# Kernel tuning notes

Measured on AMD Instinct MI355X. Metric: run time of the kernel, lower is better.

## Reference

```python
import jax, jax.numpy as jnp
import numpy as np

N = 50000        # nodes
E = 1600000      # edges (avg degree 32)
H = 128          # hidden_channels == num_filters
G = 50           # num_gaussians
L = 5            # num_interactions
CUTOFF = 4.5
VOCAB = 100
LOG2 = float(np.log(2.0))


def setup_inputs() -> dict:
    key = jax.random.key(0)
    ks = jax.random.split(key, 12)
    s = 1.0 / np.sqrt(H)
    sg = 1.0 / np.sqrt(G)
    atomic_numbers = jax.random.randint(ks[0], (N,), 0, VOCAB, dtype=jnp.int32)
    edge_index = jax.random.randint(ks[1], (2, E), 0, N, dtype=jnp.int32)
    edge_attr = jax.random.uniform(ks[2], (E,), dtype=jnp.float32)
    emb = jax.random.normal(ks[3], (VOCAB, H), dtype=jnp.float32) * 0.1
    emb = emb.at[0].set(0.0)  # padding_idx=0
    Wi = jax.random.normal(ks[4], (L, H, H), dtype=jnp.float32) * s
    bi = jnp.zeros((L, H), dtype=jnp.float32)
    Wn = jax.random.normal(ks[5], (L, G, H), dtype=jnp.float32) * sg
    bn = jnp.zeros((L, H), dtype=jnp.float32)
    Wo = jax.random.normal(ks[6], (L, H, H), dtype=jnp.float32) * s
    bo = jnp.zeros((L, H), dtype=jnp.float32)
    Wl = jax.random.normal(ks[7], (L, H, H), dtype=jnp.float32) * s
    bl = jnp.zeros((L, H), dtype=jnp.float32)
    return {"atomic_numbers": atomic_numbers, "edge_index": edge_index,
            "edge_attr": edge_attr, "emb": emb,
            "Wi": Wi, "bi": bi, "Wn": Wn, "bn": bn,
            "Wo": Wo, "bo": bo, "Wl": Wl, "bl": bl}


def _gaussian_smearing(dist):
    offsets = jnp.linspace(0.0, CUTOFF, G, dtype=jnp.float32)
    coeff = -0.5 / (offsets[1] - offsets[0]) ** 2
    return jnp.exp(coeff * (dist[:, None] - offsets[None, :]) ** 2)  # [E, G]


def reference(atomic_numbers, edge_index, edge_attr, emb,
              Wi, bi, Wn, bn, Wo, bo, Wl, bl):
    src, dst = edge_index[0], edge_index[1]
    x = emb[atomic_numbers]                      # [N, H]
    gauss = _gaussian_smearing(edge_attr)        # [E, G]
    C = 0.5 * (jnp.cos(edge_attr * jnp.pi / CUTOFF) + 1.0)  # cosine cutoff [E]
    for l in range(L):
        W = (gauss @ Wn[l] + bn[l]) * C[:, None]   # edge filters [E, H]
        h = x @ Wi[l] + bi[l]                       # [N, H]
        msg = h[src] * W                            # gather + filter [E, H]
        agg = jax.ops.segment_sum(msg, dst, num_segments=N)  # scatter-add [N, H]
        h = agg @ Wo[l] + bo[l]
        h = jax.nn.softplus(h) - LOG2               # shifted softplus
        h = h @ Wl[l] + bl[l]
        x = x + h                                   # residual
    return x
```

## Files before the change

kernel.cpp:

```cpp
#include <hip/hip_runtime.h>
#include <hip/hip_bf16.h>

#define HDIM 128
#define NG 50
#define NL 5
#define TBN 4096
#define CAP 96
#define CAPB 9000
#define CHUNK 8192

static constexpr float CUTOFF_F = 4.5f;
static constexpr float PI_F = 3.14159265358979323846f;
static constexpr float LN2_F = 0.6931471805599453f;

typedef __attribute__((ext_vector_type(8))) short bf16x8;
typedef __attribute__((ext_vector_type(4))) float f32x4;

__device__ __forceinline__ unsigned f2bfbits(float f) {
    unsigned b = __float_as_uint(f);
    return (b + 0x7FFFu + ((b >> 16) & 1u)) >> 16;
}
__device__ __forceinline__ float bflo(unsigned u) { return __uint_as_float(u << 16); }
__device__ __forceinline__ float bfhi(unsigned u) { return __uint_as_float(u & 0xFFFF0000u); }

__device__ __forceinline__ float softplus_shifted(float v) {
    return fmaxf(v, 0.0f) + log1pf(__expf(-fabsf(v))) - LN2_F;
}

__global__ __launch_bounds__(256) void embed_kernel(
    const int* __restrict__ an, const float* __restrict__ emb,
    float* __restrict__ x, int n)
{
    int idx = blockIdx.x * 256 + threadIdx.x;
    int total = n * (HDIM / 4);
    if (idx >= total) return;
    int i = idx >> 5;
    int j = idx & 31;
    int a = an[i];
    reinterpret_cast<float4*>(x)[(size_t)i * 32 + j] =
        reinterpret_cast<const float4*>(emb)[(size_t)a * 32 + j];
}

__global__ __launch_bounds__(256) void prep_weights(
    const float* __restrict__ Wi, const float* __restrict__ Wo,
    const float* __restrict__ Wl, unsigned short* __restrict__ Wt)
{
    int b = blockIdx.x;
    int l = b / 3, m = b % 3;
    const float* src = (m == 0 ? Wi : (m == 1 ? Wo : Wl)) + (size_t)l * HDIM * HDIM;
    unsigned short* dst = Wt + (size_t)b * HDIM * HDIM;
    for (int idx = threadIdx.x; idx < HDIM * HDIM; idx += 256) {
        int k = idx >> 7, n = idx & 127;
        dst[n * HDIM + k] = (unsigned short)f2bfbits(src[k * HDIM + n]);
    }
}

__global__ __launch_bounds__(128) void build_tables_all(
    const float* __restrict__ Wn, const float* __restrict__ bn,
    unsigned short* __restrict__ T)
{
    __shared__ float gs[NG];
    int p = blockIdx.x;
    int l = blockIdx.y;
    int j = threadIdx.x;
    const float* Wnl = Wn + (size_t)l * NG * HDIM;
    float d = (float)p * (1.0f / (float)TBN);
    if (j < NG) {
        const float delta = CUTOFF_F / (float)(NG - 1);
        const float coeff = -0.5f / (delta * delta);
        float t = d - (float)j * delta;
        gs[j] = expf(coeff * t * t);
    }
    __syncthreads();
    float acc = bn[(size_t)l * HDIM + j];
    #pragma unroll 10
    for (int g = 0; g < NG; ++g) acc = fmaf(gs[g], Wnl[g * HDIM + j], acc);
    acc *= 0.5f * (cosf(d * (PI_F / CUTOFF_F)) + 1.0f);
    T[((size_t)l * (TBN + 1) + p) * HDIM + j] = (unsigned short)f2bfbits(acc);
}

__global__ __launch_bounds__(512) void bucket_pass(
    const int* __restrict__ src, const int* __restrict__ dstp,
    const float* __restrict__ attr, int* __restrict__ gbase,
    uint2* __restrict__ buf, int E, int nbuck)
{
    __shared__ int hist[256], cur[256], base_l[256];
    const int tid = threadIdx.x;
    if (tid < 256) { hist[tid] = 0; cur[tid] = 0; }
    __syncthreads();
    const int e0 = blockIdx.x * CHUNK;
    const int e1 = min(e0 + CHUNK, E);
    for (int e = e0 + tid; e < e1; e += 512)
        atomicAdd(&hist[dstp[e] >> 8], 1);
    __syncthreads();
    if (tid < nbuck)
        base_l[tid] = hist[tid] ? atomicAdd(&gbase[tid], hist[tid]) : 0;
    __syncthreads();
    for (int e = e0 + tid; e < e1; e += 512) {
        int d = dstp[e];
        int b = d >> 8;
        int rank = atomicAdd(&cur[b], 1);
        int pos = base_l[b] + rank;
        unsigned ii = (unsigned)(int)fminf(attr[e] * (float)TBN + 0.5f, (float)TBN);
        if (pos < CAPB)
            buf[(size_t)b * CAPB + pos] = make_uint2((ii << 16) | (unsigned)src[e], (unsigned)d);
    }
}

__global__ __launch_bounds__(512) void bin_pass(
    const int* __restrict__ gtot, const uint2* __restrict__ buf,
    unsigned* __restrict__ sp, int* __restrict__ cnt, int N)
{
    __shared__ int cl[256];
    const int b = blockIdx.x;
    const int tid = threadIdx.x;
    if (tid < 256) cl[tid] = 0;
    __syncthreads();
    int total = gtot[b];
    if (total > CAPB) total = CAPB;
    const uint2* rb = buf + (size_t)b * CAPB;
    for (int i = tid; i < total; i += 512) {
        uint2 r = rb[i];
        int node = (int)r.y;
        int slot = atomicAdd(&cl[node & 255], 1);
        if (slot < CAP) sp[(size_t)node * CAP + slot] = r.x;
    }
    __syncthreads();
    if (tid < 256) {
        int node = b * 256 + tid;
        if (node < N) cnt[node] = min(cl[tid], CAP);
    }
}

__global__ __launch_bounds__(256) void mfma_gemm0(
    const float* __restrict__ A, const unsigned short* __restrict__ Wt,
    const float* __restrict__ bias, unsigned short* __restrict__ outp, int M)
{
    __shared__ unsigned short Al[64 * HDIM];
    __shared__ unsigned short Bl[HDIM * HDIM];
    const int tid = threadIdx.x;
    const int row0 = blockIdx.x * 64;

    #pragma unroll
    for (int it = 0; it < 8; ++it) {
        int idx = it * 256 + tid;
        int n = idx >> 4;
        int k2 = (idx & 15) * 16;
        uint4 v = reinterpret_cast<const uint4*>(Wt)[idx];
        *reinterpret_cast<uint4*>(reinterpret_cast<char*>(Bl) +
            n * 256 + (k2 ^ ((n & 7) << 4))) = v;
    }
    #pragma unroll
    for (int it = 0; it < 8; ++it) {
        int idx = it * 256 + tid;
        int r = idx >> 5;
        int k2 = (idx & 31) * 8;
        int row = row0 + r;
        float4 v = make_float4(0.f, 0.f, 0.f, 0.f);
        if (row < M) v = reinterpret_cast<const float4*>(A)[(size_t)row * 32 + (idx & 31)];
        uint2 u;
        u.x = f2bfbits(v.x) | (f2bfbits(v.y) << 16);
        u.y = f2bfbits(v.z) | (f2bfbits(v.w) << 16);
        *reinterpret_cast<uint2*>(reinterpret_cast<char*>(Al) +
            r * 256 + (k2 ^ ((r & 7) << 4))) = u;
    }
    __syncthreads();

    const int wid = tid >> 6, lane = tid & 63;
    const int wr = wid >> 1, wc = wid & 1;
    const int l15 = lane & 15, l4 = lane >> 4;

    f32x4 acc[2][4] = {};
    bf16x8 afrag[2][4];
    #pragma unroll
    for (int m = 0; m < 2; ++m)
        #pragma unroll
        for (int kc = 0; kc < 4; ++kc) {
            int r = wr * 32 + m * 16 + l15;
            int k2 = (kc * 32 + l4 * 8) * 2;
            afrag[m][kc] = *reinterpret_cast<const bf16x8*>(
                reinterpret_cast<const char*>(Al) + r * 256 + (k2 ^ ((r & 7) << 4)));
        }
    #pragma unroll
    for (int n = 0; n < 4; ++n) {
        #pragma unroll
        for (int kc = 0; kc < 4; ++kc) {
            int nn = wc * 64 + n * 16 + l15;
            int k2 = (kc * 32 + l4 * 8) * 2;
            bf16x8 bfrag = *reinterpret_cast<const bf16x8*>(
                reinterpret_cast<const char*>(Bl) + nn * 256 + (k2 ^ ((nn & 7) << 4)));
            #pragma unroll
            for (int m = 0; m < 2; ++m)
                acc[m][n] = __builtin_amdgcn_mfma_f32_16x16x32_bf16(
                    afrag[m][kc], bfrag, acc[m][n], 0, 0, 0);
        }
    }
    #pragma unroll
    for (int n = 0; n < 4; ++n) {
        int col = wc * 64 + n * 16 + l15;
        float bv = bias[col];
        #pragma unroll
        for (int m = 0; m < 2; ++m)
            #pragma unroll
            for (int r = 0; r < 4; ++r) {
                int row = row0 + wr * 32 + m * 16 + l4 * 4 + r;
                if (row >= M) continue;
                outp[(size_t)row * HDIM + col] = (unsigned short)f2bfbits(acc[m][n][r] + bv);
            }
    }
}

template<int LAST>
__global__ __launch_bounds__(256) void gemm_fused(
    const unsigned short* __restrict__ aggb, const unsigned short* __restrict__ Wot,
    const float* __restrict__ bo, const unsigned short* __restrict__ Wlt,
    const float* __restrict__ bl, float* __restrict__ x,
    const unsigned short* __restrict__ Wit, const float* __restrict__ bi_,
    unsigned short* __restrict__ hb, int M)
{
    __shared__ unsigned short Al[64 * HDIM];
    __shared__ unsigned short Bl[HDIM * HDIM];
    const int tid = threadIdx.x;
    const int row0 = blockIdx.x * 64;

    #pragma unroll
    for (int it = 0; it < 8; ++it) {
        int idx = it * 256 + tid;
        int n = idx >> 4;
        int k2 = (idx & 15) * 16;
        uint4 v = reinterpret_cast<const uint4*>(Wot)[idx];
        *reinterpret_cast<uint4*>(reinterpret_cast<char*>(Bl) +
            n * 256 + (k2 ^ ((n & 7) << 4))) = v;
    }
    #pragma unroll
    for (int it = 0; it < 4; ++it) {
        int idx = it * 256 + tid;
        int r = idx >> 4;
        int k2 = (idx & 15) * 16;
        int row = row0 + r;
        uint4 v = make_uint4(0, 0, 0, 0);
        if (row < M) v = reinterpret_cast<const uint4*>(aggb)[(size_t)row * 16 + (idx & 15)];
        *reinterpret_cast<uint4*>(reinterpret_cast<char*>(Al) +
            r * 256 + (k2 ^ ((r & 7) << 4))) = v;
    }
    __syncthreads();

    const int wid = tid >> 6, lane = tid & 63;
    const int wr = wid >> 1, wc = wid & 1;
    const int l15 = lane & 15, l4 = lane >> 4;

    uint4 wl[8];
    #pragma unroll
    for (int it = 0; it < 8; ++it) wl[it] = reinterpret_cast<const uint4*>(Wlt)[it * 256 + tid];

    f32x4 acc1[2][4] = {};
    bf16x8 afrag[2][4];
    #pragma unroll
    for (int m = 0; m < 2; ++m)
        #pragma unroll
        for (int kc = 0; kc < 4; ++kc) {
            int r = wr * 32 + m * 16 + l15;
            int k2 = (kc * 32 + l4 * 8) * 2;
            afrag[m][kc] = *reinterpret_cast<const bf16x8*>(
                reinterpret_cast<const char*>(Al) + r * 256 + (k2 ^ ((r & 7) << 4)));
        }
    #pragma unroll
    for (int n = 0; n < 4; ++n)
        #pragma unroll
        for (int kc = 0; kc < 4; ++kc) {
            int nn = wc * 64 + n * 16 + l15;
            int k2 = (kc * 32 + l4 * 8) * 2;
            bf16x8 bfrag = *reinterpret_cast<const bf16x8*>(
                reinterpret_cast<const char*>(Bl) + nn * 256 + (k2 ^ ((nn & 7) << 4)));
            #pragma unroll
            for (int m = 0; m < 2; ++m)
                acc1[m][n] = __builtin_amdgcn_mfma_f32_16x16x32_bf16(
                    afrag[m][kc], bfrag, acc1[m][n], 0, 0, 0);
        }
    __syncthreads();

    #pragma unroll
    for (int it = 0; it < 8; ++it) {
        int idx = it * 256 + tid;
        int n = idx >> 4;
        int k2 = (idx & 15) * 16;
        *reinterpret_cast<uint4*>(reinterpret_cast<char*>(Bl) +
            n * 256 + (k2 ^ ((n & 7) << 4))) = wl[it];
    }
    #pragma unroll
    for (int n = 0; n < 4; ++n) {
        int col = wc * 64 + n * 16 + l15;
        float bv = bo[col];
        #pragma unroll
        for (int m = 0; m < 2; ++m)
            #pragma unroll
            for (int r = 0; r < 4; ++r) {
                int rl = wr * 32 + m * 16 + l4 * 4 + r;
                float v = softplus_shifted(acc1[m][n][r] + bv);
                *reinterpret_cast<unsigned short*>(reinterpret_cast<char*>(Al) +
                    rl * 256 + ((2 * col) ^ ((rl & 7) << 4))) = (unsigned short)f2bfbits(v);
            }
    }
    __syncthreads();

    f32x4 acc2[2][4] = {};
    #pragma unroll
    for (int m = 0; m < 2; ++m)
        #pragma unroll
        for (int kc = 0; kc < 4; ++kc) {
            int r = wr * 32 + m * 16 + l15;
            int k2 = (kc * 32 + l4 * 8) * 2;
            afrag[m][kc] = *reinterpret_cast<const bf16x8*>(
                reinterpret_cast<const char*>(Al) + r * 256 + (k2 ^ ((r & 7) << 4)));
        }
    #pragma unroll
    for (int n = 0; n < 4; ++n)
        #pragma unroll
        for (int kc = 0; kc < 4; ++kc) {
            int nn = wc * 64 + n * 16 + l15;
            int k2 = (kc * 32 + l4 * 8) * 2;
            bf16x8 bfrag = *reinterpret_cast<const bf16x8*>(
                reinterpret_cast<const char*>(Bl) + nn * 256 + (k2 ^ ((nn & 7) << 4)));
            #pragma unroll
            for (int m = 0; m < 2; ++m)
                acc2[m][n] = __builtin_amdgcn_mfma_f32_16x16x32_bf16(
                    afrag[m][kc], bfrag, acc2[m][n], 0, 0, 0);
        }
    __syncthreads();

    uint4 w2[8];
    if (!LAST) {
        #pragma unroll
        for (int it = 0; it < 8; ++it) w2[it] = reinterpret_cast<const uint4*>(Wit)[it * 256 + tid];
    }

    #pragma unroll
    for (int n = 0; n < 4; ++n) {
        int col = wc * 64 + n * 16 + l15;
        float bv = bl[col];
        #pragma unroll
        for (int m = 0; m < 2; ++m)
            #pragma unroll
            for (int r = 0; r < 4; ++r) {
                int rl = wr * 32 + m * 16 + l4 * 4 + r;
                int row = row0 + rl;
                float v = acc2[m][n][r] + bv;
                if (row < M) {
                    float* o = x + (size_t)row * HDIM + col;
                    v += *o;
                    *o = v;
                }
                if (!LAST)
                    *reinterpret_cast<unsigned short*>(reinterpret_cast<char*>(Al) +
                        rl * 256 + ((2 * col) ^ ((rl & 7) << 4))) = (unsigned short)f2bfbits(v);
            }
    }
    if (LAST) return;

    #pragma unroll
    for (int it = 0; it < 8; ++it) {
        int idx = it * 256 + tid;
        int n = idx >> 4;
        int k2 = (idx & 15) * 16;
        *reinterpret_cast<uint4*>(reinterpret_cast<char*>(Bl) +
            n * 256 + (k2 ^ ((n & 7) << 4))) = w2[it];
    }
    __syncthreads();

    f32x4 acc3[2][4] = {};
    #pragma unroll
    for (int m = 0; m < 2; ++m)
        #pragma unroll
        for (int kc = 0; kc < 4; ++kc) {
            int r = wr * 32 + m * 16 + l15;
            int k2 = (kc * 32 + l4 * 8) * 2;
            afrag[m][kc] = *reinterpret_cast<const bf16x8*>(
                reinterpret_cast<const char*>(Al) + r * 256 + (k2 ^ ((r & 7) << 4)));
        }
    #pragma unroll
    for (int n = 0; n < 4; ++n)
        #pragma unroll
        for (int kc = 0; kc < 4; ++kc) {
            int nn = wc * 64 + n * 16 + l15;
            int k2 = (kc * 32 + l4 * 8) * 2;
            bf16x8 bfrag = *reinterpret_cast<const bf16x8*>(
                reinterpret_cast<const char*>(Bl) + nn * 256 + (k2 ^ ((nn & 7) << 4)));
            #pragma unroll
            for (int m = 0; m < 2; ++m)
                acc3[m][n] = __builtin_amdgcn_mfma_f32_16x16x32_bf16(
                    afrag[m][kc], bfrag, acc3[m][n], 0, 0, 0);
        }
    #pragma unroll
    for (int n = 0; n < 4; ++n) {
        int col = wc * 64 + n * 16 + l15;
        float bv = bi_[col];
        #pragma unroll
        for (int m = 0; m < 2; ++m)
            #pragma unroll
            for (int r = 0; r < 4; ++r) {
                int row = row0 + wr * 32 + m * 16 + l4 * 4 + r;
                if (row >= M) continue;
                hb[(size_t)row * HDIM + col] = (unsigned short)f2bfbits(acc3[m][n][r] + bv);
            }
    }
}

__global__ __launch_bounds__(256) void agg_kernel(
    const int* __restrict__ cnt, const unsigned* __restrict__ sp,
    const unsigned short* __restrict__ T,
    const unsigned* __restrict__ hb,
    unsigned* __restrict__ aggb, int n)
{
    const int lane = threadIdx.x & 63;
    int node = (blockIdx.x * 256 + threadIdx.x) >> 6;
    if (node >= n) return;

    int deg = cnt[node];
    const unsigned* recs = sp + (size_t)node * CAP;
    float ax = 0.0f, ay = 0.0f;

    int i = 0;
    for (; i + 16 <= deg; i += 16) {
        unsigned rec[16], tv[16], hv[16];
        #pragma unroll
        for (int k = 0; k < 16; ++k) rec[k] = recs[i + k];
        #pragma unroll
        for (int k = 0; k < 16; ++k) {
            tv[k] = reinterpret_cast<const unsigned*>(T + (size_t)(rec[k] >> 16) * HDIM)[lane];
            hv[k] = hb[(size_t)(rec[k] & 0xFFFFu) * 64 + lane];
        }
        #pragma unroll
        for (int k = 0; k < 16; ++k) {
            ax = fmaf(bflo(hv[k]), bflo(tv[k]), ax);
            ay = fmaf(bfhi(hv[k]), bfhi(tv[k]), ay);
        }
    }
    for (; i + 4 <= deg; i += 4) {
        unsigned rec[4], tv[4], hv[4];
        #pragma unroll
        for (int k = 0; k < 4; ++k) rec[k] = recs[i + k];
        #pragma unroll
        for (int k = 0; k < 4; ++k) {
            tv[k] = reinterpret_cast<const unsigned*>(T + (size_t)(rec[k] >> 16) * HDIM)[lane];
            hv[k] = hb[(size_t)(rec[k] & 0xFFFFu) * 64 + lane];
        }
        #pragma unroll
        for (int k = 0; k < 4; ++k) {
            ax = fmaf(bflo(hv[k]), bflo(tv[k]), ax);
            ay = fmaf(bfhi(hv[k]), bfhi(tv[k]), ay);
        }
    }
    for (; i < deg; ++i) {
        unsigned rec = recs[i];
        unsigned tvv = reinterpret_cast<const unsigned*>(T + (size_t)(rec >> 16) * HDIM)[lane];
        unsigned hvv = hb[(size_t)(rec & 0xFFFFu) * 64 + lane];
        ax = fmaf(bflo(hvv), bflo(tvv), ax);
        ay = fmaf(bfhi(hvv), bfhi(tvv), ay);
    }
    aggb[(size_t)node * 64 + lane] = f2bfbits(ax) | (f2bfbits(ay) << 16);
}

extern "C" void kernel_launch(void* const* d_in, const int* in_sizes, int n_in,
                              void* d_out, int out_size, void* d_ws, size_t ws_size,
                              hipStream_t stream)
{
    const int*   an   = (const int*)d_in[0];
    const int*   ei   = (const int*)d_in[1];
    const float* attr = (const float*)d_in[2];
    const float* emb  = (const float*)d_in[3];
    const float* Wi   = (const float*)d_in[4];
    const float* bi   = (const float*)d_in[5];
    const float* Wn   = (const float*)d_in[6];
    const float* bn   = (const float*)d_in[7];
    const float* Wo   = (const float*)d_in[8];
    const float* bo   = (const float*)d_in[9];
    const float* Wl   = (const float*)d_in[10];
    const float* bl   = (const float*)d_in[11];

    const int N = in_sizes[0];
    const int E = in_sizes[2];
    const int* srcp = ei;
    const int* dstp = ei + E;
    const int nbuck = (N + 255) >> 8;

    float* x = (float*)d_out;

    char* w = (char*)d_ws;
    unsigned*       aggb = (unsigned*)w;      w += (size_t)N * HDIM * 2;
    unsigned*       hb   = (unsigned*)w;      w += (size_t)N * HDIM * 2;
    unsigned short* T    = (unsigned short*)w; w += (size_t)NL * (TBN + 1) * HDIM * 2;
    unsigned short* Wt   = (unsigned short*)w; w += (size_t)NL * 3 * HDIM * HDIM * 2;
    int*            cnt  = (int*)w;           w += (size_t)N * 4;
    int*            gbase= (int*)w;           w += 256 * 4;
    unsigned*       sp   = (unsigned*)w;      w += (size_t)N * CAP * 4;
    uint2*          buf  = (uint2*)aggb;

    prep_weights<<<NL * 3, 256, 0, stream>>>(Wi, Wo, Wl, Wt);
    embed_kernel<<<(N * 32 + 255) / 256, 256, 0, stream>>>(an, emb, x, N);
    build_tables_all<<<dim3(TBN + 1, NL), 128, 0, stream>>>(Wn, bn, T);

    hipMemsetAsync(gbase, 0, 256 * sizeof(int), stream);
    bucket_pass<<<(E + CHUNK - 1) / CHUNK, 512, 0, stream>>>(
        srcp, dstp, attr, gbase, buf, E, nbuck);
    bin_pass<<<nbuck, 512, 0, stream>>>(gbase, buf, sp, cnt, N);

    const int gemm_grid = (N + 63) / 64;
    const int agg_grid  = (N * 64 + 255) / 256;

    mfma_gemm0<<<gemm_grid, 256, 0, stream>>>(x, Wt, bi, (unsigned short*)hb, N);

    for (int l = 0; l < NL; ++l) {
        agg_kernel<<<agg_grid, 256, 0, stream>>>(
            cnt, sp, T + (size_t)l * (TBN + 1) * HDIM, hb, aggb, N);
        if (l < NL - 1) {
            gemm_fused<0><<<gemm_grid, 256, 0, stream>>>(
                (unsigned short*)aggb, Wt + (size_t)(l * 3 + 1) * HDIM * HDIM, bo + (size_t)l * HDIM,
                Wt + (size_t)(l * 3 + 2) * HDIM * HDIM, bl + (size_t)l * HDIM, x,
                Wt + (size_t)((l + 1) * 3 + 0) * HDIM * HDIM, bi + (size_t)(l + 1) * HDIM,
                (unsigned short*)hb, N);
        } else {
            gemm_fused<1><<<gemm_grid, 256, 0, stream>>>(
                (unsigned short*)aggb, Wt + (size_t)(l * 3 + 1) * HDIM * HDIM, bo + (size_t)l * HDIM,
                Wt + (size_t)(l * 3 + 2) * HDIM * HDIM, bl + (size_t)l * HDIM, x,
                Wt, bi, (unsigned short*)hb, N);
        }
    }
}
```

Measured before the change: 808.2 us.

## Split per-node aggregation across two waves; stream GEMM weights from global

The aggregation kernel now gives each node two wavefronts, each handling half of the edge list, and combines their partial sums through shared memory. The aim is more memory-level parallelism and less latency per node, at the cost of a block barrier and smaller unroll. The GEMM kernels stop staging weight matrices in LDS and read B fragments straight from global/L2, which cuts LDS use and barriers but adds repeated global loads. Output tiles are now staged in LDS and written with coalesced 16-byte stores.

```diff
diff --git a/kernel.cpp b/kernel.cpp
--- a/kernel.cpp
+++ b/kernel.cpp
@@ -25,6 +25,11 @@
 
 __device__ __forceinline__ float softplus_shifted(float v) {
     return fmaxf(v, 0.0f) + log1pf(__expf(-fabsf(v))) - LN2_F;
+}
+
+__device__ __forceinline__ bf16x8 ldB(const unsigned short* __restrict__ W,
+                                      int nn, int kc, int l4) {
+    return *reinterpret_cast<const bf16x8*>(W + nn * HDIM + kc * 32 + l4 * 8);
 }
 
 __global__ __launch_bounds__(256) void embed_kernel(
@@ -137,19 +142,10 @@
     const float* __restrict__ bias, unsigned short* __restrict__ outp, int M)
 {
     __shared__ unsigned short Al[64 * HDIM];
-    __shared__ unsigned short Bl[HDIM * HDIM];
+    __shared__ unsigned short Hs[64 * HDIM];
     const int tid = threadIdx.x;
     const int row0 = blockIdx.x * 64;
 
-    #pragma unroll
-    for (int it = 0; it < 8; ++it) {
-        int idx = it * 256 + tid;
-        int n = idx >> 4;
-        int k2 = (idx & 15) * 16;
-        uint4 v = reinterpret_cast<const uint4*>(Wt)[idx];
-        *reinterpret_cast<uint4*>(reinterpret_cast<char*>(Bl) +
-            n * 256 + (k2 ^ ((n & 7) << 4))) = v;
-    }
     #pragma unroll
     for (int it = 0; it < 8; ++it) {
         int idx = it * 256 + tid;
@@ -182,19 +178,15 @@
                 reinterpret_cast<const char*>(Al) + r * 256 + (k2 ^ ((r & 7) << 4)));
         }
     #pragma unroll
-    for (int n = 0; n < 4; ++n) {
-        #pragma unroll
-        for (int kc = 0; kc < 4; ++kc) {
-            int nn = wc * 64 + n * 16 + l15;
-            int k2 = (kc * 32 + l4 * 8) * 2;
-            bf16x8 bfrag = *reinterpret_cast<const bf16x8*>(
-                reinterpret_cast<const char*>(Bl) + nn * 256 + (k2 ^ ((nn & 7) << 4)));
+    for (int n = 0; n < 4; ++n)
+        #pragma unroll
+        for (int kc = 0; kc < 4; ++kc) {
+            bf16x8 bfrag = ldB(Wt, wc * 64 + n * 16 + l15, kc, l4);
             #pragma unroll
             for (int m = 0; m < 2; ++m)
                 acc[m][n] = __builtin_amdgcn_mfma_f32_16x16x32_bf16(
                     afrag[m][kc], bfrag, acc[m][n], 0, 0, 0);
         }
-    }
     #pragma unroll
     for (int n = 0; n < 4; ++n) {
         int col = wc * 64 + n * 16 + l15;
@@ -203,10 +195,18 @@
         for (int m = 0; m < 2; ++m)
             #pragma unroll
             for (int r = 0; r < 4; ++r) {
-                int row = row0 + wr * 32 + m * 16 + l4 * 4 + r;
-                if (row >= M) continue;
-                outp[(size_t)row * HDIM + col] = (unsigned short)f2bfbits(acc[m][n][r] + bv);
+                int rl = wr * 32 + m * 16 + l4 * 4 + r;
+                Hs[rl * HDIM + col] = (unsigned short)f2bfbits(acc[m][n][r] + bv);
             }
+    }
+    __syncthreads();
+    #pragma unroll
+    for (int it = 0; it < 4; ++it) {
+        int e = it * 256 + tid;
+        int row = row0 + (e >> 4);
+        if (row < M)
+            reinterpret_cast<uint4*>(outp)[(size_t)row0 * 16 + e] =
+                reinterpret_cast<const uint4*>(Hs)[e];
     }
 }
 
@@ -219,19 +219,10 @@
     unsigned short* __restrict__ hb, int M)
 {
     __shared__ unsigned short Al[64 * HDIM];
-    __shared__ unsigned short Bl[HDIM * HDIM];
+    __shared__ unsigned short Hs[64 * HDIM];
     const int tid = threadIdx.x;
     const int row0 = blockIdx.x * 64;
 
-    #pragma unroll
-    for (int it = 0; it < 8; ++it) {
-        int idx = it * 256 + tid;
-        int n = idx >> 4;
-        int k2 = (idx & 15) * 16;
-        uint4 v = reinterpret_cast<const uint4*>(Wot)[idx];
-        *reinterpret_cast<uint4*>(reinterpret_cast<char*>(Bl) +
-            n * 256 + (k2 ^ ((n & 7) << 4))) = v;
-    }
     #pragma unroll
     for (int it = 0; it < 4; ++it) {
         int idx = it * 256 + tid;
@@ -249,10 +240,6 @@
     const int wr = wid >> 1, wc = wid & 1;
     const int l15 = lane & 15, l4 = lane >> 4;
 
-    uint4 wl[8];
-    #pragma unroll
-    for (int it = 0; it < 8; ++it) wl[it] = reinterpret_cast<const uint4*>(Wlt)[it * 256 + tid];
-
     f32x4 acc1[2][4] = {};
     bf16x8 afrag[2][4];
     #pragma unroll
@@ -268,10 +255,7 @@
     for (int n = 0; n < 4; ++n)
         #pragma unroll
         for (int kc = 0; kc < 4; ++kc) {
-            int nn = wc * 64 + n * 16 + l15;
-            int k2 = (kc * 32 + l4 * 8) * 2;
-            bf16x8 bfrag = *reinterpret_cast<const bf16x8*>(
-                reinterpret_cast<const char*>(Bl) + nn * 256 + (k2 ^ ((nn & 7) << 4)));
+            bf16x8 bfrag = ldB(Wot, wc * 64 + n * 16 + l15, kc, l4);
             #pragma unroll
             for (int m = 0; m < 2; ++m)
                 acc1[m][n] = __builtin_amdgcn_mfma_f32_16x16x32_bf16(
@@ -279,14 +263,6 @@
         }
     __syncthreads();
 
-    #pragma unroll
-    for (int it = 0; it < 8; ++it) {
-        int idx = it * 256 + tid;
-        int n = idx >> 4;
-        int k2 = (idx & 15) * 16;
-        *reinterpret_cast<uint4*>(reinterpret_cast<char*>(Bl) +
-            n * 256 + (k2 ^ ((n & 7) << 4))) = wl[it];
-    }
     #pragma unroll
     for (int n = 0; n < 4; ++n) {
         int col = wc * 64 + n * 16 + l15;
@@ -317,22 +293,13 @@
     for (int n = 0; n < 4; ++n)
         #pragma unroll
         for (int kc = 0; kc < 4; ++kc) {
-            int nn = wc * 64 + n * 16 + l15;
-            int k2 = (kc * 32 + l4 * 8) * 2;
-            bf16x8 bfrag = *reinterpret_cast<const bf16x8*>(
-                reinterpret_cast<const char*>(Bl) + nn * 256 + (k2 ^ ((nn & 7) << 4)));
+            bf16x8 bfrag = ldB(Wlt, wc * 64 + n * 16 + l15, kc, l4);
             #pragma unroll
             for (int m = 0; m < 2; ++m)
                 acc2[m][n] = __builtin_amdgcn_mfma_f32_16x16x32_bf16(
                     afrag[m][kc], bfrag, acc2[m][n], 0, 0, 0);
         }
     __syncthreads();
-
-    uint4 w2[8];
-    if (!LAST) {
-        #pragma unroll
-        for (int it = 0; it < 8; ++it) w2[it] = reinterpret_cast<const uint4*>(Wit)[it * 256 + tid];
-    }
 
     #pragma unroll
     for (int n = 0; n < 4; ++n) {
@@ -356,15 +323,6 @@
             }
     }
     if (LAST) return;
-
-    #pragma unroll
-    for (int it = 0; it < 8; ++it) {
-        int idx = it * 256 + tid;
-        int n = idx >> 4;
-        int k2 = (idx & 15) * 16;
-        *reinterpret_cast<uint4*>(reinterpret_cast<char*>(Bl) +
-            n * 256 + (k2 ^ ((n & 7) << 4))) = w2[it];
-    }
     __syncthreads();
 
     f32x4 acc3[2][4] = {};
@@ -381,10 +339,7 @@
     for (int n = 0; n < 4; ++n)
         #pragma unroll
         for (int kc = 0; kc < 4; ++kc) {
-            int nn = wc * 64 + n * 16 + l15;
-            int k2 = (kc * 32 + l4 * 8) * 2;
-            bf16x8 bfrag = *reinterpret_cast<const bf16x8*>(
-                reinterpret_cast<const char*>(Bl) + nn * 256 + (k2 ^ ((nn & 7) << 4)));
+            bf16x8 bfrag = ldB(Wit, wc * 64 + n * 16 + l15, kc, l4);
             #pragma unroll
             for (int m = 0; m < 2; ++m)
                 acc3[m][n] = __builtin_amdgcn_mfma_f32_16x16x32_bf16(
@@ -398,10 +353,18 @@
         for (int m = 0; m < 2; ++m)
             #pragma unroll
             for (int r = 0; r < 4; ++r) {
-                int row = row0 + wr * 32 + m * 16 + l4 * 4 + r;
-                if (row >= M) continue;
-                hb[(size_t)row * HDIM + col] = (unsigned short)f2bfbits(acc3[m][n][r] + bv);
+                int rl = wr * 32 + m * 16 + l4 * 4 + r;
+                Hs[rl * HDIM + col] = (unsigned short)f2bfbits(acc3[m][n][r] + bv);
             }
+    }
+    __syncthreads();
+    #pragma unroll
+    for (int it = 0; it < 4; ++it) {
+        int e = it * 256 + tid;
+        int row = row0 + (e >> 4);
+        if (row < M)
+            reinterpret_cast<uint4*>(hb)[(size_t)row0 * 16 + e] =
+                reinterpret_cast<const uint4*>(Hs)[e];
     }
 }
 
@@ -411,31 +374,36 @@
     const unsigned* __restrict__ hb,
     unsigned* __restrict__ aggb, int n)
 {
-    const int lane = threadIdx.x & 63;
-    int node = (blockIdx.x * 256 + threadIdx.x) >> 6;
-    if (node >= n) return;
-
-    int deg = cnt[node];
+    __shared__ float2 part[2][64];
+    const int tid = threadIdx.x;
+    const int lane = tid & 63;
+    const int wv = tid >> 6;
+    const int pair = wv >> 1, half = wv & 1;
+    const int node = blockIdx.x * 2 + pair;
+
+    int deg = (node < n) ? cnt[node] : 0;
     const unsigned* recs = sp + (size_t)node * CAP;
+    int d2 = deg >> 1;
+    int i  = half ? d2 : 0;
+    int i1 = half ? deg : d2;
     float ax = 0.0f, ay = 0.0f;
 
-    int i = 0;
-    for (; i + 16 <= deg; i += 16) {
-        unsigned rec[16], tv[16], hv[16];
-        #pragma unroll
-        for (int k = 0; k < 16; ++k) rec[k] = recs[i + k];
-        #pragma unroll
-        for (int k = 0; k < 16; ++k) {
+    for (; i + 8 <= i1; i += 8) {
+        unsigned rec[8], tv[8], hv[8];
+        #pragma unroll
+        for (int k = 0; k < 8; ++k) rec[k] = recs[i + k];
+        #pragma unroll
+        for (int k = 0; k < 8; ++k) {
             tv[k] = reinterpret_cast<const unsigned*>(T + (size_t)(rec[k] >> 16) * HDIM)[lane];
             hv[k] = hb[(size_t)(rec[k] & 0xFFFFu) * 64 + lane];
         }
         #pragma unroll
-        for (int k = 0; k < 16; ++k) {
+        for (int k = 0; k < 8; ++k) {
             ax = fmaf(bflo(hv[k]), bflo(tv[k]), ax);
             ay = fmaf(bfhi(hv[k]), bfhi(tv[k]), ay);
         }
     }
-    for (; i + 4 <= deg; i += 4) {
+    if (i + 4 <= i1) {
         unsigned rec[4], tv[4], hv[4];
         #pragma unroll
         for (int k = 0; k < 4; ++k) rec[k] = recs[i + k];
@@ -449,15 +417,23 @@
             ax = fmaf(bflo(hv[k]), bflo(tv[k]), ax);
             ay = fmaf(bfhi(hv[k]), bfhi(tv[k]), ay);
         }
-    }
-    for (; i < deg; ++i) {
+        i += 4;
+    }
+    for (; i < i1; ++i) {
         unsigned rec = recs[i];
         unsigned tvv = reinterpret_cast<const unsigned*>(T + (size_t)(rec >> 16) * HDIM)[lane];
         unsigned hvv = hb[(size_t)(rec & 0xFFFFu) * 64 + lane];
         ax = fmaf(bflo(hvv), bflo(tvv), ax);
         ay = fmaf(bfhi(hvv), bfhi(tvv), ay);
     }
-    aggb[(size_t)node * 64 + lane] = f2bfbits(ax) | (f2bfbits(ay) << 16);
+
+    if (half) part[pair][lane] = make_float2(ax, ay);
+    __syncthreads();
+    if (!half && node < n) {
+        float2 p = part[pair][lane];
+        ax += p.x; ay += p.y;
+        aggb[(size_t)node * 64 + lane] = f2bfbits(ax) | (f2bfbits(ay) << 16);
+    }
 }
 
 extern "C" void kernel_launch(void* const* d_in, const int* in_sizes, int n_in,
@@ -505,7 +481,7 @@
     bin_pass<<<nbuck, 512, 0, stream>>>(gbase, buf, sp, cnt, N);
 
     const int gemm_grid = (N + 63) / 64;
-    const int agg_grid  = (N * 64 + 255) / 256;
+    const int agg_grid  = (N + 1) / 2;
 
     mfma_gemm0<<<gemm_grid, 256, 0, stream>>>(x, Wt, bi, (unsigned short*)hb, N);
 
```

New measurement: 806.3 us. Within noise of the previous version (-0.2%).
